# Performance work log

Measured on AMD Instinct MI355X. Metric: run time of the kernel, lower is better.

Reference implementation:

```python
import jax, jax.numpy as jnp
import numpy as np


def rotate_every_two(x):
    # x: [..., d] with d even; interleave pairs (x1, x2) -> (-x2, x1)
    x1 = x[..., ::2]
    x2 = x[..., 1::2]
    return jnp.stack([-x2, x1], axis=-1).reshape(x.shape)


def theta_shift(x, sin, cos):
    return x * cos + rotate_every_two(x) * sin


def rope_2d(H, W, head_dim, dtype=jnp.float32):
    # angle: [head_dim//4] -> interleaved repeat -> [head_dim//2]
    angle = 1.0 / (10000.0 ** np.linspace(0.0, 1.0, head_dim // 4))
    angle = jnp.asarray(np.repeat(angle, 2), dtype=dtype)  # [d/2]
    ih = jnp.arange(H, dtype=dtype)[:, None] * angle[None, :]  # [H, d/2]
    iw = jnp.arange(W, dtype=dtype)[:, None] * angle[None, :]  # [W, d/2]
    sin_h = jnp.broadcast_to(jnp.sin(ih)[:, None, :], (H, W, head_dim // 2))
    sin_w = jnp.broadcast_to(jnp.sin(iw)[None, :, :], (H, W, head_dim // 2))
    cos_h = jnp.broadcast_to(jnp.cos(ih)[:, None, :], (H, W, head_dim // 2))
    cos_w = jnp.broadcast_to(jnp.cos(iw)[None, :, :], (H, W, head_dim // 2))
    sin = jnp.concatenate([sin_h, sin_w], -1).reshape(H * W, head_dim)
    cos = jnp.concatenate([cos_h, cos_w], -1).reshape(H * W, head_dim)
    return sin, cos


NUM_HEADS = 12


def setup_inputs() -> dict:
    key = jax.random.key(0)
    ks = jax.random.split(key, 11)
    B, N, C = 4, 4096, 768
    s = 1.0 / np.sqrt(C)
    return {
        "query": jax.random.normal(ks[0], (B, N, C), jnp.float32),
        "key": jax.random.normal(ks[1], (B, N, C), jnp.float32),
        "value": jax.random.normal(ks[2], (B, N, C), jnp.float32),
        "Wq": jax.random.normal(ks[3], (C, C), jnp.float32) * s,
        "bq": jax.random.normal(ks[4], (C,), jnp.float32) * s,
        "Wk": jax.random.normal(ks[5], (C, C), jnp.float32) * s,
        "bk": jax.random.normal(ks[6], (C,), jnp.float32) * s,
        "Wv": jax.random.normal(ks[7], (C, C), jnp.float32) * s,
        "bv": jax.random.normal(ks[8], (C,), jnp.float32) * s,
        "Wo": jax.random.normal(ks[9], (C, C), jnp.float32) * s,
        "bo": jax.random.normal(ks[10], (C,), jnp.float32) * s,
        "H": 64,
        "W": 64,
    }


def reference(query, key, value, Wq, bq, Wk, bk, Wv, bv, Wo, bo, H, W):
    B, N, C = query.shape
    h = NUM_HEADS
    d = C // h
    scale = d ** (-0.5)

    def heads(x):  # [B,N,C] -> [B,h,N,d]
        return x.reshape(B, N, h, d).transpose(0, 2, 1, 3)

    q = heads(query @ Wq.T + bq)
    k = heads(key @ Wk.T + bk)
    v = heads(value @ Wv.T + bv)

    q = jax.nn.elu(q) + 1.0
    k = jax.nn.elu(k) + 1.0

    sin, cos = rope_2d(H, W, d, q.dtype)  # each [N, d]

    # z: magnitude term using pre-RoPE feature maps, [B,h,N,1]
    z = jnp.einsum("bhnd,bhd->bhn", q, k.mean(axis=2))[..., None] * scale

    q = theta_shift(q, sin, cos)
    k = theta_shift(k, sin, cos)

    # linear attention: kv = k^T v scaled by scale/N, [B,h,d,d]
    kv = jnp.einsum("bhnd,bhne->bhde", k, v) * (scale / N)
    v_mean = v.mean(axis=2, keepdims=True)  # [B,h,1,d]
    res = jnp.einsum("bhnd,bhde->bhne", q, kv) * (1.0 + 1.0 / (z + 1e-6)) - z * v_mean

    res = res.transpose(0, 2, 1, 3).reshape(B, N, C)
    return res @ Wo.T + bo
```

## Files before the change

kernel.cpp:

```cpp
#include <hip/hip_runtime.h>
#include <math.h>

#define B_SZ   4
#define N_SEQ  4096
#define C_DIM  768
#define NH     12
#define HD     64
#define NBH    (B_SZ*NH)
#define SCALE  0.125f
#define M_ROWS (B_SZ*N_SEQ)

typedef unsigned short u16;
typedef short s16x8 __attribute__((ext_vector_type(8)));
typedef float f32x4 __attribute__((ext_vector_type(4)));
typedef u16 u16x8 __attribute__((ext_vector_type(8)));

__device__ __forceinline__ u16 f2h(float f) { _Float16 h = (_Float16)f; return __builtin_bit_cast(u16, h); }
__device__ __forceinline__ float h2f(u16 u) { return (float)__builtin_bit_cast(_Float16, u); }

__device__ __forceinline__ s16x8 pack_h8(f32x4 x, f32x4 y) {
    s16x8 o;
    #pragma unroll
    for (int i = 0; i < 4; ++i) { o[i] = (short)f2h(x[i]); o[i+4] = (short)f2h(y[i]); }
    return o;
}

typedef const __attribute__((address_space(1))) void GLBV;
typedef __attribute__((address_space(3))) void LDSV;
#define GLDS(g, l) __builtin_amdgcn_global_load_lds((GLBV*)(g), (LDSV*)(l), 16, 0, 0)

__global__ __launch_bounds__(256)
void cvt_w(const float* __restrict__ w0, const float* __restrict__ w1,
           const float* __restrict__ w2, const float* __restrict__ w3,
           u16* __restrict__ o0, u16* __restrict__ o1, u16* __restrict__ o2, u16* __restrict__ o3) {
    size_t i = ((size_t)blockIdx.x * 256 + threadIdx.x) * 8;
    const float* srcs[4] = {w0 + i, w1 + i, w2 + i, w3 + i};
    u16* dsts[4] = {o0 + i, o1 + i, o2 + i, o3 + i};
    #pragma unroll
    for (int s = 0; s < 4; ++s) {
        float4 x = *(const float4*)srcs[s];
        float4 y = *(const float4*)(srcs[s] + 4);
        u16x8 o;
        o[0] = f2h(x.x); o[1] = f2h(x.y); o[2] = f2h(x.z); o[3] = f2h(x.w);
        o[4] = f2h(y.x); o[5] = f2h(y.y); o[6] = f2h(y.z); o[7] = f2h(y.w);
        *(u16x8*)dsts[s] = o;
    }
}

__global__ void rope_table_k(const int* __restrict__ dH, const int* __restrict__ dW,
                             float* __restrict__ sin_t, float* __restrict__ cos_t) {
    int idx = blockIdx.x * 256 + threadIdx.x;
    if (idx >= N_SEQ * HD) return;
    int n = idx >> 6, j = idx & 63;
    int Wd = dW[0];
    int hh = n / Wd, ww = n % Wd;
    int jj = j & 31;
    float pos = (j < 32) ? (float)hh : (float)ww;
    float freq = powf(10000.0f, -((float)(jj >> 1) / 15.0f));
    float th = pos * freq;
    sin_t[idx] = sinf(th);
    cos_t[idx] = cosf(th);
}


template<int ACT>
__global__ __launch_bounds__(512)
void gemm_f32a(const float* __restrict__ A, const u16* __restrict__ Bw,
               const float* __restrict__ bias, u16* __restrict__ Cc) {
    constexpr int K = C_DIM, Nn = C_DIM;
    __shared__ __align__(16) u16 As[128 * 64];
    __shared__ __align__(16) u16 Bs[128 * 64];
    const int t = threadIdx.x;
    const int lane = t & 63, w = t >> 6;
    const int wr = w >> 1, wc = w & 1;
    const int bid = blockIdx.x;
    const int wg = (bid & 7) * 96 + (bid >> 3);
    const int bx = wg % 6, by = wg / 6;
    const int m0 = by * 128, n0 = bx * 128;

    const int ra = lane & 15, kgu = lane >> 4;

    const int srow = t >> 2, sqtr = t & 3;
    const float* gAr = A + (size_t)(m0 + srow) * K + sqtr * 16;
    u16* wA0 = &As[srow * 64 + (((sqtr * 2 + 0) ^ (srow & 7)) << 3)];
    u16* wA1 = &As[srow * 64 + (((sqtr * 2 + 1) ^ (srow & 7)) << 3)];

    const int brow = w * 8 + (lane >> 3);
    const int bcol = ((lane & 7) * 8) ^ ((lane >> 3) << 3);
    const u16* gB = Bw + (size_t)(n0 + brow) * K + bcol;

    f32x4 acc[2][4] = {};
    f32x4 pa0, pa1, pa2, pa3;
    pa0 = *(const f32x4*)(gAr + 0);
    pa1 = *(const f32x4*)(gAr + 4);
    pa2 = *(const f32x4*)(gAr + 8);
    pa3 = *(const f32x4*)(gAr + 12);

    for (int k0 = 0; k0 < K; k0 += 64) {
        __syncthreads();
        *(s16x8*)wA0 = pack_h8(pa0, pa1);
        *(s16x8*)wA1 = pack_h8(pa2, pa3);
        GLDS(gB,                  &Bs[(0 * 64 + w * 8) * 64]);
        GLDS(gB + (size_t)64 * K, &Bs[(1 * 64 + w * 8) * 64]);
        gB += 64;
        __syncthreads();
        if (k0 + 64 < K) {
            pa0 = *(const f32x4*)(gAr + k0 + 64);
            pa1 = *(const f32x4*)(gAr + k0 + 68);
            pa2 = *(const f32x4*)(gAr + k0 + 72);
            pa3 = *(const f32x4*)(gAr + k0 + 76);
        }
        #pragma unroll
        for (int kk = 0; kk < 2; ++kk) {
            const int fo = (kk * 32 + kgu * 8) ^ ((ra & 7) << 3);
            s16x8 av[2], bv[4];
            #pragma unroll
            for (int i = 0; i < 2; ++i)
                av[i] = *(const s16x8*)&As[(wr * 32 + i * 16 + ra) * 64 + fo];
            #pragma unroll
            for (int j = 0; j < 4; ++j)
                bv[j] = *(const s16x8*)&Bs[(wc * 64 + j * 16 + ra) * 64 + fo];
            #pragma unroll
            for (int i = 0; i < 2; ++i)
                #pragma unroll
                for (int j = 0; j < 4; ++j)
                    asm("v_mfma_f32_16x16x32_f16 %0, %1, %2, %0"
                        : "+v"(acc[i][j]) : "v"(av[i]), "v"(bv[j]));
        }
    }

    const int cr4 = kgu * 4, cc = ra;
    #pragma unroll
    for (int j = 0; j < 4; ++j) {
        const int col = n0 + wc * 64 + j * 16 + cc;
        const float bj = bias[col];
        #pragma unroll
        for (int i = 0; i < 2; ++i) {
            const int row = m0 + wr * 32 + i * 16 + cr4;
            #pragma unroll
            for (int r = 0; r < 4; ++r) {
                float v = acc[i][j][r] + bj;
                if (ACT) v = (v > 0.f) ? (v + 1.f) : __expf(v);
                Cc[(size_t)(row + r) * Nn + col] = f2h(v);
            }
        }
    }
}

__global__ __launch_bounds__(512)
void gemm_q(const float* __restrict__ A, const u16* __restrict__ Bw,
            const float* __restrict__ bias, const float* __restrict__ km,
            const float* __restrict__ sin_t, const float* __restrict__ cos_t,
            u16* __restrict__ Qr, float* __restrict__ zbuf) {
    constexpr int K = C_DIM, Nn = C_DIM;
    __shared__ __align__(16) u16 As[128 * 64];
    __shared__ __align__(16) u16 Bs[128 * 64];
    const int t = threadIdx.x;
    const int lane = t & 63, w = t >> 6;
    const int wr = w >> 1, wc = w & 1;
    const int bid = blockIdx.x;
    const int wg = (bid & 7) * 96 + (bid >> 3);
    const int bx = wg % 6, by = wg / 6;
    const int m0 = by * 128, n0 = bx * 128;

    const int ra = lane & 15, kgu = lane >> 4;

    const int srow = t >> 2, sqtr = t & 3;
    const float* gAr = A + (size_t)(m0 + srow) * K + sqtr * 16;
    u16* wA0 = &As[srow * 64 + (((sqtr * 2 + 0) ^ (srow & 7)) << 3)];
    u16* wA1 = &As[srow * 64 + (((sqtr * 2 + 1) ^ (srow & 7)) << 3)];

    const int brow = w * 8 + (lane >> 3);
    const int bcol = ((lane & 7) * 8) ^ ((lane >> 3) << 3);
    const u16* gB = Bw + (size_t)(n0 + brow) * K + bcol;

    f32x4 acc[2][4] = {};
    f32x4 pa0, pa1, pa2, pa3;
    pa0 = *(const f32x4*)(gAr + 0);
    pa1 = *(const f32x4*)(gAr + 4);
    pa2 = *(const f32x4*)(gAr + 8);
    pa3 = *(const f32x4*)(gAr + 12);

    for (int k0 = 0; k0 < K; k0 += 64) {
        __syncthreads();
        *(s16x8*)wA0 = pack_h8(pa0, pa1);
        *(s16x8*)wA1 = pack_h8(pa2, pa3);
        GLDS(gB,                  &Bs[(0 * 64 + w * 8) * 64]);
        GLDS(gB + (size_t)64 * K, &Bs[(1 * 64 + w * 8) * 64]);
        gB += 64;
        __syncthreads();
        if (k0 + 64 < K) {
            pa0 = *(const f32x4*)(gAr + k0 + 64);
            pa1 = *(const f32x4*)(gAr + k0 + 68);
            pa2 = *(const f32x4*)(gAr + k0 + 72);
            pa3 = *(const f32x4*)(gAr + k0 + 76);
        }
        #pragma unroll
        for (int kk = 0; kk < 2; ++kk) {
            const int fo = (kk * 32 + kgu * 8) ^ ((ra & 7) << 3);
            s16x8 av[2], bv[4];
            #pragma unroll
            for (int i = 0; i < 2; ++i)
                av[i] = *(const s16x8*)&As[(wr * 32 + i * 16 + ra) * 64 + fo];
            #pragma unroll
            for (int j = 0; j < 4; ++j)
                bv[j] = *(const s16x8*)&Bs[(wc * 64 + j * 16 + ra) * 64 + fo];
            #pragma unroll
            for (int i = 0; i < 2; ++i)
                #pragma unroll
                for (int j = 0; j < 4; ++j)
                    asm("v_mfma_f32_16x16x32_f16 %0, %1, %2, %0"
                        : "+v"(acc[i][j]) : "v"(av[i]), "v"(bv[j]));
        }
    }

    const int cr4 = kgu * 4, cc = ra;
    const int b = m0 >> 12;
    const int h = (n0 >> 6) + wc;
    float kmv[4];
    #pragma unroll
    for (int j = 0; j < 4; ++j) kmv[j] = km[(b * NH + h) * HD + j * 16 + cc];

    #pragma unroll
    for (int i = 0; i < 2; ++i) {
        #pragma unroll
        for (int r = 0; r < 4; ++r) {
            const int row = m0 + wr * 32 + i * 16 + cr4 + r;
            const int n = row & (N_SEQ - 1);
            float q[4], zp = 0.f;
            #pragma unroll
            for (int j = 0; j < 4; ++j) {
                float v = acc[i][j][r] + bias[n0 + wc * 64 + j * 16 + cc];
                v = (v > 0.f) ? (v + 1.f) : __expf(v);
                q[j] = v;
                zp += v * kmv[j];
            }
            zp += __shfl_xor(zp, 1); zp += __shfl_xor(zp, 2);
            zp += __shfl_xor(zp, 4); zp += __shfl_xor(zp, 8);
            if (cc == 0) zbuf[((size_t)(b * NH + h)) * N_SEQ + n] = zp * SCALE;
            #pragma unroll
            for (int j = 0; j < 4; ++j) {
                const int d = j * 16 + cc;
                const float p = __shfl_xor(q[j], 1);
                const float rot = (d & 1) ? p : -p;
                const size_t toff = (size_t)n * HD + d;
                const float qr = q[j] * cos_t[toff] + rot * sin_t[toff];
                Qr[(size_t)row * Nn + n0 + wc * 64 + d] = f2h(qr);
            }
        }
    }
}

__global__ __launch_bounds__(512)
void gemm_f16a(const u16* __restrict__ A, const u16* __restrict__ Bw,
               const float* __restrict__ bias, float* __restrict__ Cc) {
    constexpr int K = C_DIM, Nn = C_DIM;
    __shared__ __align__(16) u16 As[128 * 64];
    __shared__ __align__(16) u16 Bs[128 * 64];
    const int t = threadIdx.x;
    const int lane = t & 63, w = t >> 6;
    const int wr = w >> 1, wc = w & 1;
    const int bid = blockIdx.x;
    const int wg = (bid & 7) * 96 + (bid >> 3);
    const int bx = wg % 6, by = wg / 6;
    const int m0 = by * 128, n0 = bx * 128;

    const int ra = lane & 15, kgu = lane >> 4;

    const int srow = t >> 2, sqtr = t & 3;
    const u16* gAr = A + (size_t)(m0 + srow) * K + sqtr * 16;
    u16* wA0 = &As[srow * 64 + (((sqtr * 2 + 0) ^ (srow & 7)) << 3)];
    u16* wA1 = &As[srow * 64 + (((sqtr * 2 + 1) ^ (srow & 7)) << 3)];

    const int brow = w * 8 + (lane >> 3);
    const int bcol = ((lane & 7) * 8) ^ ((lane >> 3) << 3);
    const u16* gB = Bw + (size_t)(n0 + brow) * K + bcol;

    f32x4 acc[2][4] = {};
    u16x8 qa0 = *(const u16x8*)(gAr + 0);
    u16x8 qa1 = *(const u16x8*)(gAr + 8);

    for (int k0 = 0; k0 < K; k0 += 64) {
        __syncthreads();
        *(u16x8*)wA0 = qa0;
        *(u16x8*)wA1 = qa1;
        GLDS(gB,                  &Bs[(0 * 64 + w * 8) * 64]);
        GLDS(gB + (size_t)64 * K, &Bs[(1 * 64 + w * 8) * 64]);
        gB += 64;
        __syncthreads();
        if (k0 + 64 < K) {
            qa0 = *(const u16x8*)(gAr + k0 + 64);
            qa1 = *(const u16x8*)(gAr + k0 + 72);
        }
        #pragma unroll
        for (int kk = 0; kk < 2; ++kk) {
            const int fo = (kk * 32 + kgu * 8) ^ ((ra & 7) << 3);
            s16x8 av[2], bv[4];
            #pragma unroll
            for (int i = 0; i < 2; ++i)
                av[i] = *(const s16x8*)&As[(wr * 32 + i * 16 + ra) * 64 + fo];
            #pragma unroll
            for (int j = 0; j < 4; ++j)
                bv[j] = *(const s16x8*)&Bs[(wc * 64 + j * 16 + ra) * 64 + fo];
            #pragma unroll
            for (int i = 0; i < 2; ++i)
                #pragma unroll
                for (int j = 0; j < 4; ++j)
                    asm("v_mfma_f32_16x16x32_f16 %0, %1, %2, %0"
                        : "+v"(acc[i][j]) : "v"(av[i]), "v"(bv[j]));
        }
    }

    const int cr4 = kgu * 4, cc = ra;
    #pragma unroll
    for (int j = 0; j < 4; ++j) {
        const int col = n0 + wc * 64 + j * 16 + cc;
        const float bj = bias[col];
        #pragma unroll
        for (int i = 0; i < 2; ++i) {
            const int row = m0 + wr * 32 + i * 16 + cr4;
            #pragma unroll
            for (int r = 0; r < 4; ++r)
                Cc[(size_t)(row + r) * Nn + col] = acc[i][j][r] + bj;
        }
    }
}

__global__ __launch_bounds__(256)
void kv_partial(const u16* __restrict__ Kb, const u16* __restrict__ Vb,
                const float* __restrict__ sin_t, const float* __restrict__ cos_t,
                float* __restrict__ pkv, float* __restrict__ pk, float* __restrict__ pv) {
    int bh = blockIdx.x, chunk = blockIdx.y;
    int b = bh / NH, h = bh % NH;
    int t = threadIdx.x, tx = t & 15, ty = t >> 4;
    __shared__ float Kt[32][64];
    __shared__ float Vt[32][64];
    float acc[4][4] = {};
    float sk[8] = {}, sv[8] = {};
    int n0 = chunk * 128;
    int lr = t >> 3, lc = (t & 7) * 8;
    for (int nc = 0; nc < 128; nc += 32) {
        int n = n0 + nc + lr;
        size_t off = ((size_t)b * N_SEQ + n) * C_DIM + h * HD + lc;
        size_t toff = (size_t)n * HD + lc;
        u16x8 k8 = *(const u16x8*)&Kb[off];
        u16x8 v8 = *(const u16x8*)&Vb[off];
        float kf[8], vf[8];
        #pragma unroll
        for (int i = 0; i < 8; ++i) {
            kf[i] = h2f(k8[i]); vf[i] = h2f(v8[i]);
            sk[i] += kf[i]; sv[i] += vf[i];
        }
        float4 s1 = *(const float4*)&sin_t[toff];
        float4 s2 = *(const float4*)&sin_t[toff + 4];
        float4 c1 = *(const float4*)&cos_t[toff];
        float4 c2 = *(const float4*)&cos_t[toff + 4];
        float sn[8] = {s1.x, s1.y, s1.z, s1.w, s2.x, s2.y, s2.z, s2.w};
        float cs[8] = {c1.x, c1.y, c1.z, c1.w, c2.x, c2.y, c2.z, c2.w};
        float kr[8];
        #pragma unroll
        for (int e = 0; e < 8; e += 2) {
            kr[e]   = kf[e] * cs[e]     - kf[e+1] * sn[e];
            kr[e+1] = kf[e+1] * cs[e+1] + kf[e]   * sn[e+1];
        }
        __syncthreads();
        #pragma unroll
        for (int i = 0; i < 8; ++i) { Kt[lr][lc + i] = kr[i]; Vt[lr][lc + i] = vf[i]; }
        __syncthreads();
        #pragma unroll
        for (int nn = 0; nn < 32; ++nn) {
            float a[4], bb[4];
            #pragma unroll
            for (int i = 0; i < 4; ++i) a[i] = Kt[nn][ty * 4 + i];
            #pragma unroll
            for (int j = 0; j < 4; ++j) bb[j] = Vt[nn][tx * 4 + j];
            #pragma unroll
            for (int i = 0; i < 4; ++i)
                #pragma unroll
                for (int j = 0; j < 4; ++j)
                    acc[i][j] += a[i] * bb[j];
        }
    }
    size_t obase = ((size_t)bh * 32 + chunk) * 4096;
    #pragma unroll
    for (int i = 0; i < 4; ++i)
        #pragma unroll
        for (int j = 0; j < 4; ++j)
            pkv[obase + (ty * 4 + i) * 64 + (tx * 4 + j)] = acc[i][j];
    __syncthreads();
    #pragma unroll
    for (int i = 0; i < 8; ++i) { Kt[lr][lc + i] = sk[i]; Vt[lr][lc + i] = sv[i]; }
    __syncthreads();
    if (t < 64) {
        float s1 = 0.f, s2 = 0.f;
        #pragma unroll
        for (int r = 0; r < 32; ++r) { s1 += Kt[r][t]; s2 += Vt[r][t]; }
        pk[((size_t)bh * 32 + chunk) * 64 + t] = s1;
        pv[((size_t)bh * 32 + chunk) * 64 + t] = s2;
    }
}

__global__ __launch_bounds__(256)
void kvred(const float* __restrict__ pkv, const float* __restrict__ pk, const float* __restrict__ pv,
           u16* __restrict__ kvT, float* __restrict__ km, float* __restrict__ vm) {
    int bh = blockIdx.x, t = threadIdx.x;
    int u = blockIdx.y * 256 + t;
    float s = 0.f;
    for (int c = 0; c < 32; ++c) s += pkv[((size_t)bh * 32 + c) * 4096 + u];
    s *= (SCALE / N_SEQ);
    int d = u >> 6, e = u & 63;
    u16 hi = f2h(s);
    u16 lo = f2h(s - h2f(hi));
    kvT[(size_t)bh * 8192 + e * 64 + d] = hi;
    kvT[(size_t)bh * 8192 + 4096 + e * 64 + d] = lo;
    if (blockIdx.y == 0 && t < 128) {
        int which = t >> 6, lane = t & 63;
        const float* src = which ? pv : pk;
        float s2 = 0.f;
        for (int c = 0; c < 32; ++c) s2 += src[((size_t)bh * 32 + c) * 64 + lane];
        (which ? vm : km)[bh * 64 + lane] = s2 * (1.0f / N_SEQ);
    }
}

#define LDQ 72
__global__ __launch_bounds__(256)
void res_mfma(u16* __restrict__ Qr,
              const u16* __restrict__ kvT,
              const float* __restrict__ vmean, const float* __restrict__ zbuf) {
    __shared__ __align__(16) u16 qs[128 * LDQ];
    __shared__ __align__(16) u16 kvs[2][64 * LDQ];
    __shared__ float zs[128];
    __shared__ float vms[64];
    const int bh = blockIdx.x;
    const int b = bh / NH, h = bh % NH;
    const int n0 = blockIdx.y * 128;
    const int t = threadIdx.x;
    const int lane = t & 63, w = t >> 6;

    {
        const int r = t >> 2, c = (t & 3) * 16;
        #pragma unroll
        for (int p = 0; p < 2; ++p) {
            size_t g = (size_t)bh * 8192 + p * 4096 + r * 64 + c;
            *(u16x8*)&kvs[p][r * LDQ + c]     = *(const u16x8*)&kvT[g];
            *(u16x8*)&kvs[p][r * LDQ + c + 8] = *(const u16x8*)&kvT[g + 8];
        }
    }
    if (t < 64) vms[t] = vmean[bh * 64 + t];
    else if (t < 192) zs[t - 64] = zbuf[(size_t)bh * N_SEQ + n0 + (t - 64)];
    #pragma unroll
    for (int ri = 0; ri < 4; ++ri) {
        const int row = ri * 32 + (t >> 3);
        const int c = (t & 7) * 8;
        size_t off = ((size_t)b * N_SEQ + n0 + row) * C_DIM + (size_t)h * HD + c;
        *(u16x8*)&qs[row * LDQ + c] = *(const u16x8*)&Qr[off];
    }
    __syncthreads();

    f32x4 acc[2][4] = {};
    const int ra = lane & 15, kg = (lane >> 4) * 8;
    #pragma unroll
    for (int p = 0; p < 2; ++p) {
        #pragma unroll
        for (int hh = 0; hh < 2; ++hh) {
            s16x8 bv4[4];
            #pragma unroll
            for (int j = 0; j < 4; ++j)
                bv4[j] = *(const s16x8*)&kvs[p][(j * 16 + ra) * LDQ + hh * 32 + kg];
            #pragma unroll
            for (int i = 0; i < 2; ++i) {
                s16x8 av = *(const s16x8*)&qs[(w * 32 + i * 16 + ra) * LDQ + hh * 32 + kg];
                #pragma unroll
                for (int j = 0; j < 4; ++j)
                    asm("v_mfma_f32_16x16x32_f16 %0, %1, %2, %0"
                        : "+v"(acc[i][j]) : "v"(av), "v"(bv4[j]));
            }
        }
    }

    const int cr4 = (lane >> 4) * 4, cc = lane & 15;
    #pragma unroll
    for (int i = 0; i < 2; ++i) {
        #pragma unroll
        for (int j = 0; j < 4; ++j) {
            const int col = j * 16 + cc;
            const float vmc = vms[col];
            #pragma unroll
            for (int r = 0; r < 4; ++r) {
                const int row = w * 32 + i * 16 + cr4 + r;
                const float z = zs[row];
                const float v = acc[i][j][r] * (1.0f + 1.0f / (z + 1e-6f)) - z * vmc;
                Qr[((size_t)b * N_SEQ + n0 + row) * C_DIM + (size_t)h * HD + col] = f2h(v);
            }
        }
    }
}

extern "C" void kernel_launch(void* const* d_in, const int* in_sizes, int n_in,
                              void* d_out, int out_size, void* d_ws, size_t ws_size,
                              hipStream_t stream) {
    const float* query = (const float*)d_in[0];
    const float* key   = (const float*)d_in[1];
    const float* value = (const float*)d_in[2];
    const float* Wq = (const float*)d_in[3];
    const float* bq = (const float*)d_in[4];
    const float* Wk = (const float*)d_in[5];
    const float* bk = (const float*)d_in[6];
    const float* Wv = (const float*)d_in[7];
    const float* bv = (const float*)d_in[8];
    const float* Wo = (const float*)d_in[9];
    const float* bo = (const float*)d_in[10];
    const int* dH = (const int*)d_in[11];
    const int* dW = (const int*)d_in[12];
    float* out = (float*)d_out;

    const size_t mc = (size_t)M_ROWS * C_DIM;
    const size_t wsz = (size_t)C_DIM * C_DIM;

    u16* ws16 = (u16*)d_ws;
    u16* Qr  = ws16;
    u16* Kb  = Qr + mc;
    u16* Vb  = Kb + mc;
    u16* wqb = Vb + mc;
    u16* wkb = wqb + wsz;
    u16* wvb = wkb + wsz;
    u16* wob = wvb + wsz;
    u16* kvT = wob + wsz;

    float* wsf = (float*)(kvT + (size_t)NBH * 8192);
    float* sin_t = wsf;
    float* cos_t = sin_t + (size_t)N_SEQ * HD;
    float* pk    = cos_t + (size_t)N_SEQ * HD;
    float* pv    = pk + (size_t)NBH * 32 * 64;
    float* km    = pv + (size_t)NBH * 32 * 64;
    float* vm    = km + NBH * 64;
    float* zbuf  = vm + NBH * 64;
    float* pkv   = zbuf + (size_t)NBH * N_SEQ;

    cvt_w<<<dim3(288), dim3(256), 0, stream>>>(Wq, Wk, Wv, Wo, wqb, wkb, wvb, wob);
    rope_table_k<<<dim3(1024), dim3(256), 0, stream>>>(dH, dW, sin_t, cos_t);

    gemm_f32a<1><<<dim3(768), dim3(512), 0, stream>>>(key,   wkb, bk, Kb);
    gemm_f32a<0><<<dim3(768), dim3(512), 0, stream>>>(value, wvb, bv, Vb);

    kv_partial<<<dim3(NBH, 32), dim3(256), 0, stream>>>(Kb, Vb, sin_t, cos_t, pkv, pk, pv);
    kvred<<<dim3(NBH, 16), dim3(256), 0, stream>>>(pkv, pk, pv, kvT, km, vm);

    gemm_q<<<dim3(768), dim3(512), 0, stream>>>(query, wqb, bq, km, sin_t, cos_t, Qr, zbuf);

    res_mfma<<<dim3(NBH, N_SEQ / 128), dim3(256), 0, stream>>>(Qr, kvT, vm, zbuf);

    gemm_f16a<<<dim3(768), dim3(512), 0, stream>>>(Qr, wob, bo, out);
}
```

Baseline: 221.4 us.

## Load GEMM weight fragments directly from global memory into registers

The three projection GEMM kernels no longer stage the B (weight) tile through LDS with global_load_lds. Each lane now loads its MFMA B fragments straight from global memory into registers, double-buffered across the two k-halves. This removes the B shared-memory buffer and its LDS reads and halves LDS usage, which may allow more blocks per CU. The cost is that weights are no longer shared between the four waves with the same column tile, so global and L2 traffic for weights rises, and register pressure grows.

```diff
diff --git a/kernel.cpp b/kernel.cpp
--- a/kernel.cpp
+++ b/kernel.cpp
@@ -24,10 +24,6 @@
     for (int i = 0; i < 4; ++i) { o[i] = (short)f2h(x[i]); o[i+4] = (short)f2h(y[i]); }
     return o;
 }
-
-typedef const __attribute__((address_space(1))) void GLBV;
-typedef __attribute__((address_space(3))) void LDSV;
-#define GLDS(g, l) __builtin_amdgcn_global_load_lds((GLBV*)(g), (LDSV*)(l), 16, 0, 0)
 
 __global__ __launch_bounds__(256)
 void cvt_w(const float* __restrict__ w0, const float* __restrict__ w1,
@@ -69,7 +65,6 @@
                const float* __restrict__ bias, u16* __restrict__ Cc) {
     constexpr int K = C_DIM, Nn = C_DIM;
     __shared__ __align__(16) u16 As[128 * 64];
-    __shared__ __align__(16) u16 Bs[128 * 64];
     const int t = threadIdx.x;
     const int lane = t & 63, w = t >> 6;
     const int wr = w >> 1, wc = w & 1;
@@ -85,9 +80,7 @@
     u16* wA0 = &As[srow * 64 + (((sqtr * 2 + 0) ^ (srow & 7)) << 3)];
     u16* wA1 = &As[srow * 64 + (((sqtr * 2 + 1) ^ (srow & 7)) << 3)];
 
-    const int brow = w * 8 + (lane >> 3);
-    const int bcol = ((lane & 7) * 8) ^ ((lane >> 3) << 3);
-    const u16* gB = Bw + (size_t)(n0 + brow) * K + bcol;
+    const u16* gBf = Bw + (size_t)(n0 + wc * 64 + ra) * K + kgu * 8;
 
     f32x4 acc[2][4] = {};
     f32x4 pa0, pa1, pa2, pa3;
@@ -96,13 +89,15 @@
     pa2 = *(const f32x4*)(gAr + 8);
     pa3 = *(const f32x4*)(gAr + 12);
 
+    s16x8 bcur[4], bnxt[4];
+    #pragma unroll
+    for (int j = 0; j < 4; ++j)
+        bcur[j] = *(const s16x8*)(gBf + (size_t)j * 16 * K);
+
     for (int k0 = 0; k0 < K; k0 += 64) {
         __syncthreads();
         *(s16x8*)wA0 = pack_h8(pa0, pa1);
         *(s16x8*)wA1 = pack_h8(pa2, pa3);
-        GLDS(gB,                  &Bs[(0 * 64 + w * 8) * 64]);
-        GLDS(gB + (size_t)64 * K, &Bs[(1 * 64 + w * 8) * 64]);
-        gB += 64;
         __syncthreads();
         if (k0 + 64 < K) {
             pa0 = *(const f32x4*)(gAr + k0 + 64);
@@ -111,21 +106,38 @@
             pa3 = *(const f32x4*)(gAr + k0 + 76);
         }
         #pragma unroll
-        for (int kk = 0; kk < 2; ++kk) {
-            const int fo = (kk * 32 + kgu * 8) ^ ((ra & 7) << 3);
-            s16x8 av[2], bv[4];
+        for (int j = 0; j < 4; ++j)
+            bnxt[j] = *(const s16x8*)(gBf + (size_t)j * 16 * K + k0 + 32);
+        {
+            const int fo = (kgu * 8) ^ ((ra & 7) << 3);
+            s16x8 av[2];
             #pragma unroll
             for (int i = 0; i < 2; ++i)
                 av[i] = *(const s16x8*)&As[(wr * 32 + i * 16 + ra) * 64 + fo];
             #pragma unroll
+            for (int i = 0; i < 2; ++i)
+                #pragma unroll
+                for (int j = 0; j < 4; ++j)
+                    asm("v_mfma_f32_16x16x32_f16 %0, %1, %2, %0"
+                        : "+v"(acc[i][j]) : "v"(av[i]), "v"(bcur[j]));
+        }
+        if (k0 + 64 < K) {
+            #pragma unroll
             for (int j = 0; j < 4; ++j)
-                bv[j] = *(const s16x8*)&Bs[(wc * 64 + j * 16 + ra) * 64 + fo];
-            #pragma unroll
-            for (int i = 0; i < 2; ++i)
-                #pragma unroll
-                for (int j = 0; j < 4; ++j)
-                    asm("v_mfma_f32_16x16x32_f16 %0, %1, %2, %0"
-                        : "+v"(acc[i][j]) : "v"(av[i]), "v"(bv[j]));
+                bcur[j] = *(const s16x8*)(gBf + (size_t)j * 16 * K + k0 + 64);
+        }
+        {
+            const int fo = (32 + kgu * 8) ^ ((ra & 7) << 3);
+            s16x8 av[2];
+            #pragma unroll
+            for (int i = 0; i < 2; ++i)
+                av[i] = *(const s16x8*)&As[(wr * 32 + i * 16 + ra) * 64 + fo];
+            #pragma unroll
+            for (int i = 0; i < 2; ++i)
+                #pragma unroll
+                for (int j = 0; j < 4; ++j)
+                    asm("v_mfma_f32_16x16x32_f16 %0, %1, %2, %0"
+                        : "+v"(acc[i][j]) : "v"(av[i]), "v"(bnxt[j]));
         }
     }
 
@@ -154,7 +166,6 @@
             u16* __restrict__ Qr, float* __restrict__ zbuf) {
     constexpr int K = C_DIM, Nn = C_DIM;
     __shared__ __align__(16) u16 As[128 * 64];
-    __shared__ __align__(16) u16 Bs[128 * 64];
     const int t = threadIdx.x;
     const int lane = t & 63, w = t >> 6;
     const int wr = w >> 1, wc = w & 1;
@@ -170,9 +181,7 @@
     u16* wA0 = &As[srow * 64 + (((sqtr * 2 + 0) ^ (srow & 7)) << 3)];
     u16* wA1 = &As[srow * 64 + (((sqtr * 2 + 1) ^ (srow & 7)) << 3)];
 
-    const int brow = w * 8 + (lane >> 3);
-    const int bcol = ((lane & 7) * 8) ^ ((lane >> 3) << 3);
-    const u16* gB = Bw + (size_t)(n0 + brow) * K + bcol;
+    const u16* gBf = Bw + (size_t)(n0 + wc * 64 + ra) * K + kgu * 8;
 
     f32x4 acc[2][4] = {};
     f32x4 pa0, pa1, pa2, pa3;
@@ -181,13 +190,15 @@
     pa2 = *(const f32x4*)(gAr + 8);
     pa3 = *(const f32x4*)(gAr + 12);
 
+    s16x8 bcur[4], bnxt[4];
+    #pragma unroll
+    for (int j = 0; j < 4; ++j)
+        bcur[j] = *(const s16x8*)(gBf + (size_t)j * 16 * K);
+
     for (int k0 = 0; k0 < K; k0 += 64) {
         __syncthreads();
         *(s16x8*)wA0 = pack_h8(pa0, pa1);
         *(s16x8*)wA1 = pack_h8(pa2, pa3);
-        GLDS(gB,                  &Bs[(0 * 64 + w * 8) * 64]);
-        GLDS(gB + (size_t)64 * K, &Bs[(1 * 64 + w * 8) * 64]);
-        gB += 64;
         __syncthreads();
         if (k0 + 64 < K) {
             pa0 = *(const f32x4*)(gAr + k0 + 64);
@@ -196,21 +207,38 @@
             pa3 = *(const f32x4*)(gAr + k0 + 76);
         }
         #pragma unroll
-        for (int kk = 0; kk < 2; ++kk) {
-            const int fo = (kk * 32 + kgu * 8) ^ ((ra & 7) << 3);
-            s16x8 av[2], bv[4];
+        for (int j = 0; j < 4; ++j)
+            bnxt[j] = *(const s16x8*)(gBf + (size_t)j * 16 * K + k0 + 32);
+        {
+            const int fo = (kgu * 8) ^ ((ra & 7) << 3);
+            s16x8 av[2];
             #pragma unroll
             for (int i = 0; i < 2; ++i)
                 av[i] = *(const s16x8*)&As[(wr * 32 + i * 16 + ra) * 64 + fo];
             #pragma unroll
+            for (int i = 0; i < 2; ++i)
+                #pragma unroll
+                for (int j = 0; j < 4; ++j)
+                    asm("v_mfma_f32_16x16x32_f16 %0, %1, %2, %0"
+                        : "+v"(acc[i][j]) : "v"(av[i]), "v"(bcur[j]));
+        }
+        if (k0 + 64 < K) {
+            #pragma unroll
             for (int j = 0; j < 4; ++j)
-                bv[j] = *(const s16x8*)&Bs[(wc * 64 + j * 16 + ra) * 64 + fo];
-            #pragma unroll
-            for (int i = 0; i < 2; ++i)
-                #pragma unroll
-                for (int j = 0; j < 4; ++j)
-                    asm("v_mfma_f32_16x16x32_f16 %0, %1, %2, %0"
-                        : "+v"(acc[i][j]) : "v"(av[i]), "v"(bv[j]));
+                bcur[j] = *(const s16x8*)(gBf + (size_t)j * 16 * K + k0 + 64);
+        }
+        {
+            const int fo = (32 + kgu * 8) ^ ((ra & 7) << 3);
+            s16x8 av[2];
+            #pragma unroll
+            for (int i = 0; i < 2; ++i)
+                av[i] = *(const s16x8*)&As[(wr * 32 + i * 16 + ra) * 64 + fo];
+            #pragma unroll
+            for (int i = 0; i < 2; ++i)
+                #pragma unroll
+                for (int j = 0; j < 4; ++j)
+                    asm("v_mfma_f32_16x16x32_f16 %0, %1, %2, %0"
+                        : "+v"(acc[i][j]) : "v"(av[i]), "v"(bnxt[j]));
         }
     }
 
@@ -256,7 +284,6 @@
                const float* __restrict__ bias, float* __restrict__ Cc) {
     constexpr int K = C_DIM, Nn = C_DIM;
     __shared__ __align__(16) u16 As[128 * 64];
-    __shared__ __align__(16) u16 Bs[128 * 64];
     const int t = threadIdx.x;
     const int lane = t & 63, w = t >> 6;
     const int wr = w >> 1, wc = w & 1;
@@ -272,42 +299,59 @@
     u16* wA0 = &As[srow * 64 + (((sqtr * 2 + 0) ^ (srow & 7)) << 3)];
     u16* wA1 = &As[srow * 64 + (((sqtr * 2 + 1) ^ (srow & 7)) << 3)];
 
-    const int brow = w * 8 + (lane >> 3);
-    const int bcol = ((lane & 7) * 8) ^ ((lane >> 3) << 3);
-    const u16* gB = Bw + (size_t)(n0 + brow) * K + bcol;
+    const u16* gBf = Bw + (size_t)(n0 + wc * 64 + ra) * K + kgu * 8;
 
     f32x4 acc[2][4] = {};
     u16x8 qa0 = *(const u16x8*)(gAr + 0);
     u16x8 qa1 = *(const u16x8*)(gAr + 8);
 
+    s16x8 bcur[4], bnxt[4];
+    #pragma unroll
+    for (int j = 0; j < 4; ++j)
+        bcur[j] = *(const s16x8*)(gBf + (size_t)j * 16 * K);
+
     for (int k0 = 0; k0 < K; k0 += 64) {
         __syncthreads();
         *(u16x8*)wA0 = qa0;
         *(u16x8*)wA1 = qa1;
-        GLDS(gB,                  &Bs[(0 * 64 + w * 8) * 64]);
-        GLDS(gB + (size_t)64 * K, &Bs[(1 * 64 + w * 8) * 64]);
-        gB += 64;
         __syncthreads();
         if (k0 + 64 < K) {
             qa0 = *(const u16x8*)(gAr + k0 + 64);
             qa1 = *(const u16x8*)(gAr + k0 + 72);
         }
         #pragma unroll
-        for (int kk = 0; kk < 2; ++kk) {
-            const int fo = (kk * 32 + kgu * 8) ^ ((ra & 7) << 3);
-            s16x8 av[2], bv[4];
+        for (int j = 0; j < 4; ++j)
+            bnxt[j] = *(const s16x8*)(gBf + (size_t)j * 16 * K + k0 + 32);
+        {
+            const int fo = (kgu * 8) ^ ((ra & 7) << 3);
+            s16x8 av[2];
             #pragma unroll
             for (int i = 0; i < 2; ++i)
                 av[i] = *(const s16x8*)&As[(wr * 32 + i * 16 + ra) * 64 + fo];
             #pragma unroll
+            for (int i = 0; i < 2; ++i)
+                #pragma unroll
+                for (int j = 0; j < 4; ++j)
+                    asm("v_mfma_f32_16x16x32_f16 %0, %1, %2, %0"
+                        : "+v"(acc[i][j]) : "v"(av[i]), "v"(bcur[j]));
+        }
+        if (k0 + 64 < K) {
+            #pragma unroll
             for (int j = 0; j < 4; ++j)
-                bv[j] = *(const s16x8*)&Bs[(wc * 64 + j * 16 + ra) * 64 + fo];
-            #pragma unroll
-            for (int i = 0; i < 2; ++i)
-                #pragma unroll
-                for (int j = 0; j < 4; ++j)
-                    asm("v_mfma_f32_16x16x32_f16 %0, %1, %2, %0"
-                        : "+v"(acc[i][j]) : "v"(av[i]), "v"(bv[j]));
+                bcur[j] = *(const s16x8*)(gBf + (size_t)j * 16 * K + k0 + 64);
+        }
+        {
+            const int fo = (32 + kgu * 8) ^ ((ra & 7) << 3);
+            s16x8 av[2];
+            #pragma unroll
+            for (int i = 0; i < 2; ++i)
+                av[i] = *(const s16x8*)&As[(wr * 32 + i * 16 + ra) * 64 + fo];
+            #pragma unroll
+            for (int i = 0; i < 2; ++i)
+                #pragma unroll
+                for (int j = 0; j < 4; ++j)
+                    asm("v_mfma_f32_16x16x32_f16 %0, %1, %2, %0"
+                        : "+v"(acc[i][j]) : "v"(av[i]), "v"(bnxt[j]));
         }
     }
 
```

Result: slower. 423.8 us (+91.4%).
